# Kernel optimization log

Measured on AMD Instinct MI355X. Metric: run time of the kernel, lower is better.

Reference implementation:

```python
import jax, jax.numpy as jnp
import numpy as np

B, T, C = 1, 4096, 1024
N_HEAD = 16
HEAD_DIM = C // N_HEAD
SCALE = 1.0 / np.sqrt(HEAD_DIM).astype(np.float32)


def setup_inputs() -> dict:
    key = jax.random.key(0)
    k1, k2, k3 = jax.random.split(key, 3)
    x = jax.random.normal(k1, (B, T, C), dtype=jnp.float32)
    W_attn = jax.random.normal(k2, (C, 3 * C), dtype=jnp.float32) * 0.02
    b_attn = jnp.zeros((3 * C,), dtype=jnp.float32)
    W_proj = jax.random.normal(k3, (C, C), dtype=jnp.float32) * 0.02
    b_proj = jnp.zeros((C,), dtype=jnp.float32)
    return {"x": x, "W_attn": W_attn, "b_attn": b_attn, "W_proj": W_proj, "b_proj": b_proj}


def reference(x, W_attn, b_attn, W_proj, b_proj):
    Bq, Tq, Cq = x.shape
    qkv = x @ W_attn + b_attn                      # [B, T, 3C]
    q, k, v = jnp.split(qkv, 3, axis=-1)
    # split heads -> [B, H, T, D]
    def split_heads(t):
        return t.reshape(Bq, Tq, N_HEAD, HEAD_DIM).transpose(0, 2, 1, 3)
    q, k, v = split_heads(q), split_heads(k), split_heads(v)
    scores = jnp.einsum('bhqd,bhkd->bhqk', q, k) * SCALE  # [B, H, T, T]
    causal = jnp.tril(jnp.ones((Tq, Tq), dtype=bool))
    scores = jnp.where(causal[None, None], scores, jnp.float32(-jnp.inf))
    probs = jax.nn.softmax(scores, axis=-1)
    out = jnp.einsum('bhqk,bhkd->bhqd', probs, v)          # [B, H, T, D]
    out = out.transpose(0, 2, 1, 3).reshape(Bq, Tq, Cq)    # merge heads
    out = out @ W_proj + b_proj
    return out
```

## Files before the change

### kernel.cpp

```cpp
#include <hip/hip_runtime.h>
#include <hip/hip_bf16.h>


typedef unsigned short u16;
typedef u16 u16x4 __attribute__((ext_vector_type(4)));
typedef u16 u16x8 __attribute__((ext_vector_type(8)));
typedef __bf16 bf16x8 __attribute__((ext_vector_type(8)));
typedef float f32x4 __attribute__((ext_vector_type(4)));

#define T_SEQ 4096
#define C_DIM 1024
#define NH 16
#define HD 64
#define QSC 0.18033688f
#define NJOBS 1152

static __device__ __forceinline__ u16 f2bf(float f) {
    __hip_bfloat16 h = __float2bfloat16(f);
    return __builtin_bit_cast(u16, h);
}

static __device__ __forceinline__ float bf2f(u16 u) {
    return __builtin_bit_cast(float, (unsigned)u << 16);
}

static __device__ __forceinline__ bf16x8 ldfr(const u16* base, int byteoff) {
    return __builtin_bit_cast(bf16x8, *(const u16x8*)(base + (byteoff >> 1)));
}

static __device__ __forceinline__ void gld_lds16(const void* g, void* l) {
    __builtin_amdgcn_global_load_lds((const __attribute__((address_space(1))) void*)g,
                                     (__attribute__((address_space(3))) void*)l, 16, 0, 0);
}

#define MFMA16(a, b, c) __builtin_amdgcn_mfma_f32_16x16x32_bf16((a), (b), (c), 0, 0, 0)


__global__ __launch_bounds__(256) void k_cvt_x(const float* __restrict__ x, u16* __restrict__ xb) {
    int i = (blockIdx.x * 256 + threadIdx.x) * 8;
    float4 a = *(const float4*)(x + i);
    float4 b = *(const float4*)(x + i + 4);
    u16x8 o;
    o[0] = f2bf(a.x); o[1] = f2bf(a.y); o[2] = f2bf(a.z); o[3] = f2bf(a.w);
    o[4] = f2bf(b.x); o[5] = f2bf(b.y); o[6] = f2bf(b.z); o[7] = f2bf(b.w);
    *(u16x8*)(xb + i) = o;
}

__global__ __launch_bounds__(256) void k_transpose_w(const float* __restrict__ src,
                                                     u16* __restrict__ dst, int R, int Cc) {
    __shared__ float tile[32][33];
    int bx = blockIdx.x * 32;
    int by = blockIdx.y * 32;
    int x = threadIdx.x, y = threadIdx.y;
#pragma unroll
    for (int i = 0; i < 32; i += 8)
        tile[y + i][x] = src[(by + y + i) * Cc + bx + x];
    __syncthreads();
#pragma unroll
    for (int i = 0; i < 32; i += 8)
        dst[(bx + y + i) * R + by + x] = f2bf(tile[x][y + i]);
}


template <int EPI>
__global__ __launch_bounds__(256) void k_gemm(const u16* __restrict__ A, const u16* __restrict__ Bt,
                                              const float* __restrict__ bias,
                                              u16* __restrict__ outQ, u16* __restrict__ outK,
                                              u16* __restrict__ outVt, float* __restrict__ outF,
                                              int kd, int nbx) {
    __shared__ u16 Al[128 * 64];
    __shared__ u16 Bl[128 * 64];
    const int tid = threadIdx.x;
    const int lane = tid & 63;
    const int wid = tid >> 6;
    const int wm = wid >> 1, wn = wid & 1;
    const int c = lane & 15, g = lane >> 4;
    const int nwg = gridDim.x;
    const int swzb = ((int)blockIdx.x & 7) * (nwg >> 3) + ((int)blockIdx.x >> 3);
    const int m0 = (swzb % nbx) * 128;
    const int n0 = (swzb / nbx) * 128;
    const int srow = lane >> 3;
    const int sxu = (((lane & 7) * 16) ^ (srow << 4)) >> 1;
    const int swa = (c & 7) << 4;

    f32x4 acc[4][4] = {};

    for (int k0 = 0; k0 < kd; k0 += 64) {
#pragma unroll
        for (int i = 0; i < 4; ++i) {
            const int ch = wid * 4 + i;
            const int row = ch * 8 + srow;
            gld_lds16(A + (m0 + row) * kd + k0 + sxu, &Al[ch * 512]);
            gld_lds16(Bt + (n0 + row) * kd + k0 + sxu, &Bl[ch * 512]);
        }
        __syncthreads();
        bf16x8 af[4][2], bfm[4][2];
#pragma unroll
        for (int mi = 0; mi < 4; ++mi) {
            const u16* p = Al + (wm * 64 + mi * 16 + c) * 64;
            af[mi][0] = ldfr(p, (16 * g) ^ swa);
            af[mi][1] = ldfr(p, (64 + 16 * g) ^ swa);
        }
#pragma unroll
        for (int ni = 0; ni < 4; ++ni) {
            const u16* p = Bl + (wn * 64 + ni * 16 + c) * 64;
            bfm[ni][0] = ldfr(p, (16 * g) ^ swa);
            bfm[ni][1] = ldfr(p, (64 + 16 * g) ^ swa);
        }
#pragma unroll
        for (int mi = 0; mi < 4; ++mi)
#pragma unroll
            for (int ni = 0; ni < 4; ++ni) {
                acc[mi][ni] = MFMA16(af[mi][0], bfm[ni][0], acc[mi][ni]);
                acc[mi][ni] = MFMA16(af[mi][1], bfm[ni][1], acc[mi][ni]);
            }
        __syncthreads();
    }

    const int mbase = m0 + wm * 64;
    const int nbase = n0 + wn * 64;
    if (EPI == 0) {
        const int part = m0 >> 10;
#pragma unroll
        for (int mi = 0; mi < 4; ++mi) {
            const int fbase = mbase + mi * 16 + 4 * g;
            const f32x4 bv = *(const f32x4*)(bias + fbase);
            const int fr = fbase & 1023;
            const int h = fr >> 6, d0 = fr & 63;
#pragma unroll
            for (int ni = 0; ni < 4; ++ni) {
                const int tok = nbase + ni * 16 + c;
                if (part == 2) {
#pragma unroll
                    for (int r = 0; r < 4; ++r)
                        outVt[(size_t)(fr + r) * T_SEQ + tok] = f2bf(acc[mi][ni][r] + bv[r]);
                } else {
                    u16x4 pk;
#pragma unroll
                    for (int r = 0; r < 4; ++r) {
                        float v = acc[mi][ni][r] + bv[r];
                        pk[r] = f2bf(part == 0 ? v * QSC : v);
                    }
                    u16* dst = (part == 0 ? outQ : outK);
                    *(u16x4*)(dst + (size_t)(h * T_SEQ + tok) * HD + d0) = pk;
                }
            }
        }
    } else {
#pragma unroll
        for (int mi = 0; mi < 4; ++mi) {
            const int fbase = mbase + mi * 16 + 4 * g;
            const f32x4 bv = *(const f32x4*)(bias + fbase);
#pragma unroll
            for (int ni = 0; ni < 4; ++ni) {
                const int tok = nbase + ni * 16 + c;
                f32x4 w;
#pragma unroll
                for (int r = 0; r < 4; ++r) w[r] = acc[mi][ni][r] + bv[r];
                *(f32x4*)(outF + (size_t)tok * C_DIM + fbase) = w;
            }
        }
    }
}


static __device__ __forceinline__ void p_gen(f32x4 s[4], int qabs, int kv0, int g,
                                             bool domask, bf16x8 pa[2]) {
    if (domask) {
#pragma unroll
        for (int tau = 0; tau < 4; ++tau) {
            const int kb = kv0 + 32 * (tau >> 1) + 4 * (tau & 1) + 8 * g;
#pragma unroll
            for (int r = 0; r < 4; ++r)
                if (kb + r > qabs) s[tau][r] = -3e38f;
        }
    }
    u16 pb[4][4];
#pragma unroll
    for (int tau = 0; tau < 4; ++tau)
#pragma unroll
        for (int r = 0; r < 4; ++r)
            pb[tau][r] = f2bf(__builtin_amdgcn_exp2f(s[tau][r]));
    const u16x8 p0 = {pb[0][0], pb[0][1], pb[0][2], pb[0][3], pb[1][0], pb[1][1], pb[1][2], pb[1][3]};
    const u16x8 p1 = {pb[2][0], pb[2][1], pb[2][2], pb[2][3], pb[3][0], pb[3][1], pb[3][2], pb[3][3]};
    pa[0] = __builtin_bit_cast(bf16x8, p0);
    pa[1] = __builtin_bit_cast(bf16x8, p1);
}

__global__ __launch_bounds__(512) void k_flash(const u16* __restrict__ Qg, const u16* __restrict__ Kg,
                                               const u16* __restrict__ Vtg, u16* __restrict__ Ab,
                                               u16* __restrict__ part, float* __restrict__ lpart,
                                               unsigned* __restrict__ cnt) {
    __shared__ u16 sm[2][2][4096];
    volatile unsigned* jw = (volatile unsigned*)&sm[0][0][0];

    const int tid = threadIdx.x;
    const int lane = tid & 63;
    const int wid = tid >> 6;
    const int c = lane & 15, g = lane >> 4;
    const int srow = lane >> 3;
    const int sxu = (((lane & 7) * 16) ^ (srow << 4)) >> 1;

    const u16x8 onespat = {0x3F80, 0x3F80, 0x3F80, 0x3F80, 0x3F80, 0x3F80, 0x3F80, 0x3F80};
    const bf16x8 onesf = __builtin_bit_cast(bf16x8, onespat);

    for (;;) {
        if (tid == 0) *jw = atomicAdd(cnt, 1u);
        __syncthreads();
        const unsigned j = *jw;
        __syncthreads();
        if (j >= (unsigned)NJOBS) break;

        const int head = (int)(j & 15u);
        const int idx = (int)(j >> 4);
        int qb, ch, nc;
        if (idx < 16)      { qb = 15 - (idx >> 3); ch = idx & 7; nc = 8; }
        else if (idx < 30) { const int t = idx - 16; qb = 13 - t / 7;    ch = t % 7; nc = 7; }
        else if (idx < 42) { const int t = idx - 30; qb = 11 - t / 6;    ch = t % 6; nc = 6; }
        else if (idx < 52) { const int t = idx - 42; qb = 9 - t / 5;     ch = t % 5; nc = 5; }
        else if (idx < 60) { const int t = idx - 52; qb = 7 - (t >> 2);  ch = t & 3; nc = 4; }
        else if (idx < 66) { const int t = idx - 60; qb = 5 - t / 3;     ch = t % 3; nc = 3; }
        else if (idx < 70) { const int t = idx - 66; qb = 3 - (t >> 1);  ch = t & 1; nc = 2; }
        else               { qb = 1 - (idx - 70); ch = 0; nc = 1; }
        const int ntile = 4 * qb + 4;
        const int cbase = ntile / nc, crem = ntile % nc;
        const int len = cbase + (ch < crem ? 1 : 0);
        const int start = ch * cbase + (ch < crem ? ch : crem);

        const int q0w = qb * 256 + wid * 32;

        const u16* Qh = Qg + (size_t)head * (T_SEQ * HD);
        const u16* Kh = Kg + (size_t)head * (T_SEQ * HD);
        const u16* Vh = Vtg + (size_t)head * (HD * T_SEQ);

        bf16x8 qf[2][2];
#pragma unroll
        for (int h = 0; h < 2; ++h)
#pragma unroll
            for (int dc = 0; dc < 2; ++dc)
                qf[h][dc] = __builtin_bit_cast(
                    bf16x8, *(const u16x8*)(Qh + (q0w + 16 * h + c) * HD + dc * 32 + 8 * g));

        f32x4 o0[4] = {}, o1[4] = {}, ol0 = {}, ol1 = {};

        {
            const int kvs = start * 64;
            gld_lds16(Kh + (kvs + wid * 8 + srow) * HD + sxu, &sm[0][0][wid * 512]);
            gld_lds16(Vh + (wid * 8 + srow) * T_SEQ + kvs + sxu, &sm[0][1][wid * 512]);
        }
        __syncthreads();

        for (int t = 0; t < len; ++t) {
            const int cur = t & 1;
            const int kv0 = (start + t) * 64;
            if (t + 1 < len) {
                const int kvn = kv0 + 64;
                gld_lds16(Kh + (kvn + wid * 8 + srow) * HD + sxu, &sm[cur ^ 1][0][wid * 512]);
                gld_lds16(Vh + (wid * 8 + srow) * T_SEQ + kvn + sxu, &sm[cur ^ 1][1][wid * 512]);
            }
            if (kv0 <= q0w + 31) {
                const u16* Kl = &sm[cur][0][0];
                const u16* Vl = &sm[cur][1][0];
                f32x4 s0[4], s1[4];
                __builtin_amdgcn_s_setprio(1);
#pragma unroll
                for (int tau = 0; tau < 4; ++tau) {
                    const int prow = 32 * (tau >> 1) + 4 * (tau & 1) + 8 * (c >> 2) + (c & 3);
                    const int sw = (prow & 7) << 4;
                    const u16* kb = Kl + prow * 64;
                    const bf16x8 k0 = ldfr(kb, (16 * g) ^ sw);
                    const bf16x8 k1 = ldfr(kb, (64 + 16 * g) ^ sw);
                    f32x4 z0 = {}, z1 = {};
                    z0 = MFMA16(k0, qf[0][0], z0);
                    s0[tau] = MFMA16(k1, qf[0][1], z0);
                    z1 = MFMA16(k0, qf[1][0], z1);
                    s1[tau] = MFMA16(k1, qf[1][1], z1);
                }
                __builtin_amdgcn_s_setprio(0);
                const bool dm0 = (kv0 + 63) > (q0w);
                const bool dm1 = (kv0 + 63) > (q0w + 16);
                bf16x8 pa0[2], pa1[2];
                p_gen(s0, q0w + c, kv0, g, dm0, pa0);
                p_gen(s1, q0w + 16 + c, kv0, g, dm1, pa1);
                const int swv = (c & 7) << 4;
                __builtin_amdgcn_s_setprio(1);
#pragma unroll
                for (int n = 0; n < 4; ++n) {
                    const u16* vb = Vl + (n * 16 + c) * 64;
                    const bf16x8 v0 = ldfr(vb, (16 * g) ^ swv);
                    const bf16x8 v1 = ldfr(vb, (64 + 16 * g) ^ swv);
                    o0[n] = MFMA16(v0, pa0[0], o0[n]);
                    o0[n] = MFMA16(v1, pa0[1], o0[n]);
                    o1[n] = MFMA16(v0, pa1[0], o1[n]);
                    o1[n] = MFMA16(v1, pa1[1], o1[n]);
                }
                ol0 = MFMA16(onesf, pa0[0], ol0);
                ol0 = MFMA16(onesf, pa0[1], ol0);
                ol1 = MFMA16(onesf, pa1[0], ol1);
                ol1 = MFMA16(onesf, pa1[1], ol1);
                __builtin_amdgcn_s_setprio(0);
            }
            __syncthreads();
        }

        const int ql0 = wid * 32 + c;
        if (nc == 1) {
            const float li0 = 1.0f / ol0[0], li1 = 1.0f / ol1[0];
            u16* dst0 = Ab + (size_t)(qb * 256 + ql0) * C_DIM + head * HD;
            u16* dst1 = dst0 + (size_t)16 * C_DIM;
#pragma unroll
            for (int n = 0; n < 4; ++n) {
                u16x4 w0, w1;
#pragma unroll
                for (int r = 0; r < 4; ++r) {
                    w0[r] = f2bf(o0[n][r] * li0);
                    w1[r] = f2bf(o1[n][r] * li1);
                }
                *(u16x4*)(dst0 + n * 16 + 4 * g) = w0;
                *(u16x4*)(dst1 + n * 16 + 4 * g) = w1;
            }
        } else {
            u16* slot = part + (size_t)j * 16384u;
            float* lsl = lpart + (size_t)j * 256u;
#pragma unroll
            for (int n = 0; n < 4; ++n) {
                u16x4 w0, w1;
#pragma unroll
                for (int r = 0; r < 4; ++r) {
                    w0[r] = f2bf(o0[n][r]);
                    w1[r] = f2bf(o1[n][r]);
                }
                *(u16x4*)(slot + ql0 * 64 + n * 16 + 4 * g) = w0;
                *(u16x4*)(slot + (ql0 + 16) * 64 + n * 16 + 4 * g) = w1;
            }
            if (g == 0) {
                lsl[ql0] = ol0[0];
                lsl[ql0 + 16] = ol1[0];
            }
        }
        __syncthreads();
    }
}


__global__ __launch_bounds__(512) void k_combine(const u16* __restrict__ part,
                                                 const float* __restrict__ lpart,
                                                 u16* __restrict__ Ab) {
    const int head = blockIdx.x / 14;
    const int qb = 2 + (blockIdx.x % 14);
    int nc, idx0;
    if (qb >= 14)      { nc = 8; idx0 = (15 - qb) * 8; }
    else if (qb >= 12) { nc = 7; idx0 = 16 + (13 - qb) * 7; }
    else if (qb >= 10) { nc = 6; idx0 = 30 + (11 - qb) * 6; }
    else if (qb >= 8)  { nc = 5; idx0 = 42 + (9 - qb) * 5; }
    else if (qb >= 6)  { nc = 4; idx0 = 52 + (7 - qb) * 4; }
    else if (qb >= 4)  { nc = 3; idx0 = 60 + (5 - qb) * 3; }
    else               { nc = 2; idx0 = 66 + (3 - qb) * 2; }

    const int q = threadIdx.x >> 1;
    const int dh = (threadIdx.x & 1) * 32;
    float acc[32] = {};
    float l = 0.f;
    for (int i = 0; i < nc; ++i) {
        const unsigned jj = (unsigned)(((idx0 + i) << 4) | head);
        const u16* sp = part + (size_t)jj * 16384u + q * 64 + dh;
#pragma unroll
        for (int v = 0; v < 4; ++v) {
            const u16x8 w = *(const u16x8*)(sp + 8 * v);
#pragma unroll
            for (int e = 0; e < 8; ++e) acc[8 * v + e] += bf2f(w[e]);
        }
        l += lpart[(size_t)jj * 256u + q];
    }
    const float li = 1.0f / l;
    u16* dst = Ab + (size_t)(qb * 256 + q) * C_DIM + head * HD + dh;
#pragma unroll
    for (int v = 0; v < 4; ++v) {
        u16x8 w;
#pragma unroll
        for (int e = 0; e < 8; ++e) w[e] = f2bf(acc[8 * v + e] * li);
        *(u16x8*)(dst + 8 * v) = w;
    }
}


extern "C" void kernel_launch(void* const* d_in, const int* in_sizes, int n_in,
                              void* d_out, int out_size, void* d_ws, size_t ws_size,
                              hipStream_t stream) {
    const float* x      = (const float*)d_in[0];
    const float* W_attn = (const float*)d_in[1];
    const float* b_attn = (const float*)d_in[2];
    const float* W_proj = (const float*)d_in[3];
    const float* b_proj = (const float*)d_in[4];
    float* out = (float*)d_out;

    char* ws = (char*)d_ws;
    u16* xb    = (u16*)(ws);
    u16* Wat   = (u16*)(ws + (8u << 20));
    u16* Wpt   = (u16*)(ws + (14u << 20));
    u16* Qb    = (u16*)(ws + (16u << 20));
    u16* Kb    = (u16*)(ws + (24u << 20));
    u16* Vtb   = (u16*)(ws + (32u << 20));
    u16* prt   = (u16*)(ws + (40u << 20));
    float* lpt = (float*)(ws + (78u << 20));
    u16* Ab    = xb;

    unsigned* cnt = (unsigned*)d_out;
    hipMemsetAsync(cnt, 0, 4, stream);

    k_cvt_x<<<2048, 256, 0, stream>>>(x, xb);
    k_transpose_w<<<dim3(96, 32), dim3(32, 8), 0, stream>>>(W_attn, Wat, 1024, 3072);
    k_transpose_w<<<dim3(32, 32), dim3(32, 8), 0, stream>>>(W_proj, Wpt, 1024, 1024);
    k_gemm<0><<<768, 256, 0, stream>>>(Wat, xb, b_attn, Qb, Kb, Vtb, nullptr, 1024, 24);
    k_flash<<<512, 512, 0, stream>>>(Qb, Kb, Vtb, Ab, prt, lpt, cnt);
    k_combine<<<224, 512, 0, stream>>>(prt, lpt, Ab);
    k_gemm<1><<<256, 256, 0, stream>>>(Wpt, Ab, b_proj, nullptr, nullptr, nullptr, out, 1024, 8);
}
```

Baseline: 165.4 us.

## Deepen K/V LDS pipeline to four stages with vmcnt-based waits

New measurement: 158.6 us. 1.04x faster.

```diff
diff --git a/kernel.cpp b/kernel.cpp
--- a/kernel.cpp
+++ b/kernel.cpp
@@ -187,12 +187,12 @@
     pa[1] = __builtin_bit_cast(bf16x8, p1);
 }
 
-__global__ __launch_bounds__(512) void k_flash(const u16* __restrict__ Qg, const u16* __restrict__ Kg,
-                                               const u16* __restrict__ Vtg, u16* __restrict__ Ab,
-                                               u16* __restrict__ part, float* __restrict__ lpart,
-                                               unsigned* __restrict__ cnt) {
-    __shared__ u16 sm[2][2][4096];
-    volatile unsigned* jw = (volatile unsigned*)&sm[0][0][0];
+__global__ __launch_bounds__(512, 4) void k_flash(const u16* __restrict__ Qg, const u16* __restrict__ Kg,
+                                                  const u16* __restrict__ Vtg, u16* __restrict__ Ab,
+                                                  u16* __restrict__ part, float* __restrict__ lpart,
+                                                  unsigned* __restrict__ cnt) {
+    __shared__ u16 sm[4][2][4096];
+    __shared__ unsigned jslot;
 
     const int tid = threadIdx.x;
     const int lane = tid & 63;
@@ -205,10 +205,9 @@
     const bf16x8 onesf = __builtin_bit_cast(bf16x8, onespat);
 
     for (;;) {
-        if (tid == 0) *jw = atomicAdd(cnt, 1u);
+        if (tid == 0) jslot = atomicAdd(cnt, 1u);
         __syncthreads();
-        const unsigned j = *jw;
-        __syncthreads();
+        const unsigned j = jslot;
         if (j >= (unsigned)NJOBS) break;
 
         const int head = (int)(j & 15u);
@@ -243,24 +242,27 @@
 
         f32x4 o0[4] = {}, o1[4] = {}, ol0 = {}, ol1 = {};
 
-        {
-            const int kvs = start * 64;
-            gld_lds16(Kh + (kvs + wid * 8 + srow) * HD + sxu, &sm[0][0][wid * 512]);
-            gld_lds16(Vh + (wid * 8 + srow) * T_SEQ + kvs + sxu, &sm[0][1][wid * 512]);
-        }
-        __syncthreads();
+#pragma unroll
+        for (int i = 0; i < 3; ++i) {
+            const int ts = (i < len ? start + i : start + len - 1) * 64;
+            gld_lds16(Kh + (ts + wid * 8 + srow) * HD + sxu, &sm[i][0][wid * 512]);
+            gld_lds16(Vh + (wid * 8 + srow) * T_SEQ + ts + sxu, &sm[i][1][wid * 512]);
+        }
 
         for (int t = 0; t < len; ++t) {
-            const int cur = t & 1;
+            asm volatile("s_waitcnt vmcnt(4)" ::: "memory");
+            __builtin_amdgcn_s_barrier();
+            __builtin_amdgcn_sched_barrier(0);
+            {
+                const int ts = (t + 3 < len ? start + t + 3 : start + len - 1) * 64;
+                const int sl = (t + 3) & 3;
+                gld_lds16(Kh + (ts + wid * 8 + srow) * HD + sxu, &sm[sl][0][wid * 512]);
+                gld_lds16(Vh + (wid * 8 + srow) * T_SEQ + ts + sxu, &sm[sl][1][wid * 512]);
+            }
             const int kv0 = (start + t) * 64;
-            if (t + 1 < len) {
-                const int kvn = kv0 + 64;
-                gld_lds16(Kh + (kvn + wid * 8 + srow) * HD + sxu, &sm[cur ^ 1][0][wid * 512]);
-                gld_lds16(Vh + (wid * 8 + srow) * T_SEQ + kvn + sxu, &sm[cur ^ 1][1][wid * 512]);
-            }
             if (kv0 <= q0w + 31) {
-                const u16* Kl = &sm[cur][0][0];
-                const u16* Vl = &sm[cur][1][0];
+                const u16* Kl = &sm[t & 3][0][0];
+                const u16* Vl = &sm[t & 3][1][0];
                 f32x4 s0[4], s1[4];
                 __builtin_amdgcn_s_setprio(1);
 #pragma unroll
@@ -300,7 +302,6 @@
                 ol1 = MFMA16(onesf, pa1[1], ol1);
                 __builtin_amdgcn_s_setprio(0);
             }
-            __syncthreads();
         }
 
         const int ql0 = wid * 32 + c;
```
